# Kernel tuning notes

Hardware: AMD Instinct MI355X
Metric: run time of the kernel (lower is better)

## Reference

```python
import jax, jax.numpy as jnp
import numpy as np

N = 50000      # nodes per type (tx and addr)
E = 400000     # edges per relation
IN, H, OUT = 128, 256, 2
RELS = ['tt', 'aa', 'at', 'ta']


def setup_inputs() -> dict:
    key = jax.random.key(0)
    ks = jax.random.split(key, 32)
    inp = {}
    inp['x_tx'] = jax.random.normal(ks[0], (N, IN), jnp.float32)
    inp['x_addr'] = jax.random.normal(ks[1], (N, IN), jnp.float32)
    for i, r in enumerate(RELS):
        inp['e_' + r] = jax.random.randint(ks[2 + i], (2, E), 0, N, jnp.int32)
    k = 6
    for li, (din, dout) in enumerate([(IN, H), (H, OUT)]):
        for r in RELS:
            inp[f'Wl{li}_{r}'] = jax.random.normal(ks[k], (dout, din), jnp.float32) * 0.05; k += 1
            inp[f'bl{li}_{r}'] = jnp.zeros((dout,), jnp.float32)
            inp[f'Wr{li}_{r}'] = jax.random.normal(ks[k], (dout, din), jnp.float32) * 0.05; k += 1
    return inp


def _sage(x_src, x_dst, edge, Wl, bl, Wr):
    # PyG SAGEConv: lin_l(mean_{j in N(i)} x_j) + lin_r(x_i)
    n = x_dst.shape[0]
    msg = x_src[edge[0]]                                         # [E, d] gather
    s = jax.ops.segment_sum(msg, edge[1], num_segments=n)        # [n, d] scatter-add
    cnt = jax.ops.segment_sum(jnp.ones((edge.shape[1],), x_src.dtype), edge[1], num_segments=n)
    agg = s / jnp.maximum(cnt, 1.0)[:, None]                     # mean (0 for isolated)
    return agg @ Wl.T + bl + x_dst @ Wr.T


def reference(x_tx, x_addr, e_tt, e_aa, e_at, e_ta,
              Wl0_tt, bl0_tt, Wr0_tt, Wl0_aa, bl0_aa, Wr0_aa,
              Wl0_at, bl0_at, Wr0_at, Wl0_ta, bl0_ta, Wr0_ta,
              Wl1_tt, bl1_tt, Wr1_tt, Wl1_aa, bl1_aa, Wr1_aa,
              Wl1_at, bl1_at, Wr1_at, Wl1_ta, bl1_ta, Wr1_ta):
    # Layer 0: HeteroConv with aggr='sum' over relations per destination type
    h_tx = _sage(x_tx, x_tx, e_tt, Wl0_tt, bl0_tt, Wr0_tt) + \
           _sage(x_addr, x_tx, e_at, Wl0_at, bl0_at, Wr0_at)
    h_ad = _sage(x_addr, x_addr, e_aa, Wl0_aa, bl0_aa, Wr0_aa) + \
           _sage(x_tx, x_addr, e_ta, Wl0_ta, bl0_ta, Wr0_ta)
    h_tx = jax.nn.relu(h_tx)   # dropout is identity at inference
    h_ad = jax.nn.relu(h_ad)
    # Layer 1 (output)
    o_tx = _sage(h_tx, h_tx, e_tt, Wl1_tt, bl1_tt, Wr1_tt) + \
           _sage(h_ad, h_tx, e_at, Wl1_at, bl1_at, Wr1_at)
    o_ad = _sage(h_ad, h_ad, e_aa, Wl1_aa, bl1_aa, Wr1_aa) + \
           _sage(h_tx, h_ad, e_ta, Wl1_ta, bl1_ta, Wr1_ta)
    return o_tx, o_ad
```

## Files before the change

### kernel.cpp

```cpp
#include <hip/hip_runtime.h>
#include <hip/hip_fp8.h>


#define DIN 128
#define DH  256
#define LDSA 136
#define LDSH 264

typedef __attribute__((ext_vector_type(8))) short bf16x8;
typedef __attribute__((ext_vector_type(4))) float f32x4;
typedef __attribute__((ext_vector_type(2))) float f32x2;

__device__ __forceinline__ unsigned short f2bf(float f) {
    unsigned int u = __float_as_uint(f);
    u = (u + 0x7fffu + ((u >> 16) & 1u)) >> 16;
    return (unsigned short)u;
}

#if __has_builtin(__builtin_amdgcn_cvt_pk_fp8_f32) && __has_builtin(__builtin_amdgcn_cvt_pk_f32_fp8)
__device__ __forceinline__ unsigned pk_fp8(float4 a) {
    unsigned v = (unsigned)__builtin_amdgcn_cvt_pk_fp8_f32(a.x, a.y, 0, false);
    v = (unsigned)__builtin_amdgcn_cvt_pk_fp8_f32(a.z, a.w, (int)v, true);
    return v;
}
__device__ __forceinline__ void acc_fp8x4(float* a, unsigned u) {
    f32x2 f0 = __builtin_amdgcn_cvt_pk_f32_fp8((int)u, false);
    f32x2 f1 = __builtin_amdgcn_cvt_pk_f32_fp8((int)u, true);
    a[0] += f0.x; a[1] += f0.y; a[2] += f1.x; a[3] += f1.y;
}
#else
__device__ __forceinline__ unsigned pk_fp8(float4 a) {
    __hip_fp8_e4m3 v0(a.x), v1(a.y), v2(a.z), v3(a.w);
    return (unsigned)v0.__x | ((unsigned)v1.__x << 8) |
           ((unsigned)v2.__x << 16) | ((unsigned)v3.__x << 24);
}
__device__ __forceinline__ void acc_fp8x4(float* a, unsigned u) {
    __hip_fp8_e4m3 v0, v1, v2, v3;
    v0.__x = (unsigned char)(u & 0xff);
    v1.__x = (unsigned char)((u >> 8) & 0xff);
    v2.__x = (unsigned char)((u >> 16) & 0xff);
    v3.__x = (unsigned char)((u >> 24) & 0xff);
    a[0] += (float)v0; a[1] += (float)v1; a[2] += (float)v2; a[3] += (float)v3;
}
#endif

__device__ __forceinline__ void acc_fp8x16(float* a, uint4 u) {
    acc_fp8x4(a + 0,  u.x);
    acc_fp8x4(a + 4,  u.y);
    acc_fp8x4(a + 8,  u.z);
    acc_fp8x4(a + 12, u.w);
}

__global__ __launch_bounds__(256) void setup_kernel(
    const float* __restrict__ x_tx, const float* __restrict__ x_addr,
    const float* __restrict__ Wl0_tt, const float* __restrict__ Wl0_aa,
    const float* __restrict__ Wl0_at, const float* __restrict__ Wl0_ta,
    const float* __restrict__ Wr0_tt, const float* __restrict__ Wr0_aa,
    const float* __restrict__ Wr0_at, const float* __restrict__ Wr0_ta,
    const float* __restrict__ bl0_tt, const float* __restrict__ bl0_aa,
    const float* __restrict__ bl0_at, const float* __restrict__ bl0_ta,
    const float* __restrict__ Wl1_tt, const float* __restrict__ Wl1_aa,
    const float* __restrict__ Wl1_at, const float* __restrict__ Wl1_ta,
    const float* __restrict__ Wr1_tt, const float* __restrict__ Wr1_aa,
    const float* __restrict__ Wr1_at, const float* __restrict__ Wr1_ta,
    const float* __restrict__ bl1_tt, const float* __restrict__ bl1_aa,
    const float* __restrict__ bl1_at, const float* __restrict__ bl1_ta,
    unsigned short* __restrict__ xb_tx, unsigned short* __restrict__ xb_ad,
    uint2* __restrict__ x8_tx, uint2* __restrict__ x8_ad,
    unsigned short* __restrict__ wb_tt, unsigned short* __restrict__ wb_aa,
    unsigned short* __restrict__ wb_at, unsigned short* __restrict__ wb_ta,
    unsigned short* __restrict__ wr0c_tx, unsigned short* __restrict__ wr0c_ad,
    float* __restrict__ b0c, unsigned short* __restrict__ wzb,
    float* __restrict__ b1c, int N)
{
    int i = blockIdx.x * blockDim.x + threadIdx.x;
    int nconv = N * DIN / 8;
    if (i < nconv) {
        {
            const float4* p = (const float4*)(x_tx + (size_t)i * 8);
            float4 a = p[0], b = p[1];
            uint4 o;
            o.x = (unsigned)f2bf(a.x) | ((unsigned)f2bf(a.y) << 16);
            o.y = (unsigned)f2bf(a.z) | ((unsigned)f2bf(a.w) << 16);
            o.z = (unsigned)f2bf(b.x) | ((unsigned)f2bf(b.y) << 16);
            o.w = (unsigned)f2bf(b.z) | ((unsigned)f2bf(b.w) << 16);
            *(uint4*)(xb_tx + (size_t)i * 8) = o;
            x8_tx[i] = make_uint2(pk_fp8(a), pk_fp8(b));
        }
        {
            const float4* p = (const float4*)(x_addr + (size_t)i * 8);
            float4 a = p[0], b = p[1];
            uint4 o;
            o.x = (unsigned)f2bf(a.x) | ((unsigned)f2bf(a.y) << 16);
            o.y = (unsigned)f2bf(a.z) | ((unsigned)f2bf(a.w) << 16);
            o.z = (unsigned)f2bf(b.x) | ((unsigned)f2bf(b.y) << 16);
            o.w = (unsigned)f2bf(b.z) | ((unsigned)f2bf(b.w) << 16);
            *(uint4*)(xb_ad + (size_t)i * 8) = o;
            x8_ad[i] = make_uint2(pk_fp8(a), pk_fp8(b));
        }
    }
    if (i < DH * DIN) {
        wb_tt[i] = f2bf(Wl0_tt[i]);
        wb_aa[i] = f2bf(Wl0_aa[i]);
        wb_at[i] = f2bf(Wl0_at[i]);
        wb_ta[i] = f2bf(Wl0_ta[i]);
        wr0c_tx[i] = f2bf(Wr0_tt[i] + Wr0_at[i]);
        wr0c_ad[i] = f2bf(Wr0_aa[i] + Wr0_ta[i]);
    }
    if (i < DH) {
        b0c[i]      = bl0_tt[i] + bl0_at[i];
        b0c[DH + i] = bl0_aa[i] + bl0_ta[i];
    }
    if (i < 2 * 16 * DH) {
        int type = i >> 12;
        int rem = i & 4095;
        int r = rem >> 8;
        int c = rem & 255;
        float v = 0.f;
        if (r < 6) {
            const float* A = type ? Wl1_aa : Wl1_tt;
            const float* B = type ? Wl1_at : Wl1_ta;
            if (r == 0) v = A[c];
            else if (r == 1) v = A[DH + c];
            else if (r == 2) v = B[c];
            else if (r == 3) v = B[DH + c];
            else if (r == 4) v = type ? (Wr1_aa[c] + Wr1_ta[c]) : (Wr1_tt[c] + Wr1_at[c]);
            else             v = type ? (Wr1_aa[DH + c] + Wr1_ta[DH + c])
                                      : (Wr1_tt[DH + c] + Wr1_at[DH + c]);
        }
        wzb[i] = f2bf(v);
    }
    if (i < 2) {
        b1c[i]     = bl1_tt[i] + bl1_at[i];
        b1c[2 + i] = bl1_aa[i] + bl1_ta[i];
    }
}

__global__ __launch_bounds__(256) void bhist_kernel(
    const int* __restrict__ e0, const int* __restrict__ e1,
    const int* __restrict__ e2, const int* __restrict__ e3,
    int* __restrict__ bcnt, int E, int nb)
{
    int r = blockIdx.y;
    const int* e = (r == 0) ? e0 : (r == 1) ? e1 : (r == 2) ? e2 : e3;
    __shared__ int h[256];
    if (threadIdx.x < nb) h[threadIdx.x] = 0;
    __syncthreads();
    int base = (blockIdx.x * 256 + threadIdx.x) * 16;
    if (base + 16 <= E) {
        const int4* p = (const int4*)(e + E + base);
        int4 d0 = p[0], d1 = p[1], d2 = p[2], d3 = p[3];
        atomicAdd(&h[(unsigned)d0.x >> 8], 1); atomicAdd(&h[(unsigned)d0.y >> 8], 1);
        atomicAdd(&h[(unsigned)d0.z >> 8], 1); atomicAdd(&h[(unsigned)d0.w >> 8], 1);
        atomicAdd(&h[(unsigned)d1.x >> 8], 1); atomicAdd(&h[(unsigned)d1.y >> 8], 1);
        atomicAdd(&h[(unsigned)d1.z >> 8], 1); atomicAdd(&h[(unsigned)d1.w >> 8], 1);
        atomicAdd(&h[(unsigned)d2.x >> 8], 1); atomicAdd(&h[(unsigned)d2.y >> 8], 1);
        atomicAdd(&h[(unsigned)d2.z >> 8], 1); atomicAdd(&h[(unsigned)d2.w >> 8], 1);
        atomicAdd(&h[(unsigned)d3.x >> 8], 1); atomicAdd(&h[(unsigned)d3.y >> 8], 1);
        atomicAdd(&h[(unsigned)d3.z >> 8], 1); atomicAdd(&h[(unsigned)d3.w >> 8], 1);
    } else {
        for (int i = base; i < E; ++i)
            atomicAdd(&h[(unsigned)e[E + i] >> 8], 1);
    }
    __syncthreads();
    if (threadIdx.x < nb) {
        int v = h[threadIdx.x];
        if (v) atomicAdd(&bcnt[r * nb + threadIdx.x], v);
    }
}

__global__ __launch_bounds__(1024) void bscan_kernel(
    const int* __restrict__ bcnt, int* __restrict__ bbase, int* __restrict__ bcur, int n)
{
    __shared__ int s[1024];
    int t = threadIdx.x;
    int v = (t < n) ? bcnt[t] : 0;
    s[t] = v;
    __syncthreads();
    for (int off = 1; off < 1024; off <<= 1) {
        int x = (t >= off) ? s[t - off] : 0;
        __syncthreads();
        s[t] += x;
        __syncthreads();
    }
    if (t < n) {
        int ex = s[t] - v;
        bbase[t] = ex;
        bcur[t] = ex;
    }
    if (t == 0) bbase[n] = s[1023];
}

__global__ __launch_bounds__(256) void bscatter_kernel(
    const int* __restrict__ e0, const int* __restrict__ e1,
    const int* __restrict__ e2, const int* __restrict__ e3,
    int* __restrict__ bcur, unsigned* __restrict__ tmp, int E, int nb)
{
    int r = blockIdx.y;
    const int* e = (r == 0) ? e0 : (r == 1) ? e1 : (r == 2) ? e2 : e3;
    __shared__ int h[256];
    __shared__ int lbase[256];
    __shared__ int lcur[256];
    if (threadIdx.x < nb) { h[threadIdx.x] = 0; lcur[threadIdx.x] = 0; }
    __syncthreads();
    int base = (blockIdx.x * 256 + threadIdx.x) * 16;
    int dst[16], src[16];
    int cnt16 = 0;
    if (base + 16 <= E) {
        const int4* pd = (const int4*)(e + E + base);
        const int4* ps = (const int4*)(e + base);
#pragma unroll
        for (int j = 0; j < 4; ++j) {
            int4 d = pd[j], s4 = ps[j];
            dst[j * 4 + 0] = d.x; dst[j * 4 + 1] = d.y; dst[j * 4 + 2] = d.z; dst[j * 4 + 3] = d.w;
            src[j * 4 + 0] = s4.x; src[j * 4 + 1] = s4.y; src[j * 4 + 2] = s4.z; src[j * 4 + 3] = s4.w;
        }
        cnt16 = 16;
    } else {
        for (int i = base; i < E; ++i) {
            dst[cnt16] = e[E + i];
            src[cnt16] = e[i];
            ++cnt16;
        }
    }
    for (int j = 0; j < cnt16; ++j)
        atomicAdd(&h[(unsigned)dst[j] >> 8], 1);
    __syncthreads();
    if (threadIdx.x < nb) {
        int c = h[threadIdx.x];
        if (c) lbase[threadIdx.x] = atomicAdd(&bcur[r * nb + threadIdx.x], c);
    }
    __syncthreads();
    for (int j = 0; j < cnt16; ++j) {
        int bk = (unsigned)dst[j] >> 8;
        int rank = atomicAdd(&lcur[bk], 1);
        tmp[lbase[bk] + rank] =
            (((unsigned)dst[j] & 255u) << 16) | (unsigned)src[j];
    }
}

__global__ __launch_bounds__(256) void bgroup_kernel(
    const unsigned* __restrict__ tmp, const int* __restrict__ bbase,
    int* __restrict__ col, int* __restrict__ rowptr, int* __restrict__ cnt,
    int N, int nb)
{
    int b = blockIdx.x;
    int r = blockIdx.y;
    int idx = r * nb + b;
    int lo = bbase[idx], hi = bbase[idx + 1];
    __shared__ int h[256];
    __shared__ int cur[256];
    __shared__ int exs[256];
    int t = threadIdx.x;
    h[t] = 0; cur[t] = 0;
    __syncthreads();
    for (int i = lo + t; i < hi; i += 256)
        atomicAdd(&h[(tmp[i] >> 16) & 255u], 1);
    __syncthreads();
    {
        __shared__ int s[256];
        int v = h[t];
        s[t] = v;
        __syncthreads();
        for (int off = 1; off < 256; off <<= 1) {
            int x = (t >= off) ? s[t - off] : 0;
            __syncthreads();
            s[t] += x;
            __syncthreads();
        }
        exs[t] = s[t] - v;
    }
    __syncthreads();
    int d = b * 256 + t;
    if (d < N) {
        rowptr[r * N + d] = lo + exs[t];
        cnt[r * N + d] = h[t];
    }
    for (int i = lo + t; i < hi; i += 256) {
        unsigned p = tmp[i];
        int fine = (p >> 16) & 255u;
        int rank = atomicAdd(&cur[fine], 1);
        col[lo + exs[fine] + rank] = (int)(p & 0xffffu);
    }
}

__global__ __launch_bounds__(256) void agg_kernel(
    const uint4* __restrict__ x8_tx, const uint4* __restrict__ x8_ad,
    const int* __restrict__ rowptr, const int* __restrict__ cnt,
    const int* __restrict__ col, unsigned short* __restrict__ aggb, int N)
{
    int r = blockIdx.y;
    const uint4* xs = (r == 0 || r == 3) ? x8_tx : x8_ad;
    int t = threadIdx.x;
    int wv = t >> 6;
    int l  = t & 63;
    int oct = l >> 3;
    int d   = l & 7;
    int node = blockIdx.x * 32 + wv * 8 + oct;
    if (node >= N) return;
    int idx = r * N + node;
    int base = rowptr[idx];
    int c    = cnt[idx];
    const int* cl = col + base;
    float a0[16] = {}, a1[16] = {};
    int e = 0;
    for (; e + 2 <= c; e += 2) {
        int s0 = cl[e];
        int s1 = cl[e + 1];
        uint4 u0 = xs[((unsigned)s0 << 3) + d];
        uint4 u1 = xs[((unsigned)s1 << 3) + d];
        acc_fp8x16(a0, u0);
        acc_fp8x16(a1, u1);
    }
    if (e < c) {
        int s0 = cl[e];
        uint4 u0 = xs[((unsigned)s0 << 3) + d];
        acc_fp8x16(a0, u0);
    }
    float sc = 1.0f / fmaxf((float)c, 1.0f);
    uint4 o0, o1;
    o0.x = (unsigned)f2bf((a0[0] + a1[0]) * sc)  | ((unsigned)f2bf((a0[1] + a1[1]) * sc) << 16);
    o0.y = (unsigned)f2bf((a0[2] + a1[2]) * sc)  | ((unsigned)f2bf((a0[3] + a1[3]) * sc) << 16);
    o0.z = (unsigned)f2bf((a0[4] + a1[4]) * sc)  | ((unsigned)f2bf((a0[5] + a1[5]) * sc) << 16);
    o0.w = (unsigned)f2bf((a0[6] + a1[6]) * sc)  | ((unsigned)f2bf((a0[7] + a1[7]) * sc) << 16);
    o1.x = (unsigned)f2bf((a0[8] + a1[8]) * sc)  | ((unsigned)f2bf((a0[9] + a1[9]) * sc) << 16);
    o1.y = (unsigned)f2bf((a0[10] + a1[10]) * sc) | ((unsigned)f2bf((a0[11] + a1[11]) * sc) << 16);
    o1.z = (unsigned)f2bf((a0[12] + a1[12]) * sc) | ((unsigned)f2bf((a0[13] + a1[13]) * sc) << 16);
    o1.w = (unsigned)f2bf((a0[14] + a1[14]) * sc) | ((unsigned)f2bf((a0[15] + a1[15]) * sc) << 16);
    uint4* orow = (uint4*)(aggb + ((size_t)r * N + node) * DIN);
    orow[d * 2]     = o0;
    orow[d * 2 + 1] = o1;
}

__global__ __launch_bounds__(256) void gemm0z_kernel(
    const unsigned short* __restrict__ xb_tx, const unsigned short* __restrict__ xb_ad,
    const unsigned short* __restrict__ aggb,
    const unsigned short* __restrict__ wb_tt, const unsigned short* __restrict__ wb_at,
    const unsigned short* __restrict__ wr0c_tx,
    const unsigned short* __restrict__ wb_aa, const unsigned short* __restrict__ wb_ta,
    const unsigned short* __restrict__ wr0c_ad,
    const float* __restrict__ b0c, const unsigned short* __restrict__ wzb,
    const float* __restrict__ b1c,
    float* __restrict__ z, float* __restrict__ outp, int N)
{
    __shared__ unsigned short lds[3 * 64 * LDSA];
    const int type = blockIdx.y;
    const unsigned short* xself = type ? xb_ad : xb_tx;
    const unsigned short* A0 = aggb + (size_t)(type ? 1 : 0) * N * DIN;
    const unsigned short* A1 = aggb + (size_t)(type ? 3 : 2) * N * DIN;
    const unsigned short* W0 = type ? wb_aa   : wb_tt;
    const unsigned short* W1 = type ? wb_ta   : wb_at;
    const unsigned short* W2 = type ? wr0c_ad : wr0c_tx;
    const float* bias = b0c + type * DH;
    float* zA = type ? (z + (size_t)1 * N * 2) : z;
    float* zB = type ? (z + (size_t)2 * N * 2) : (z + (size_t)3 * N * 2);
    float* outSelf = outp + (size_t)type * N * 2;

    const int t  = threadIdx.x;
    const int wv = t >> 6;
    const int l  = t & 63;
    const int q  = l >> 4;
    const int lr = l & 15;
    const int m0 = blockIdx.x * 64;
    const int n0 = wv * 64;

    {
        const uint4* As[3] = {(const uint4*)A0, (const uint4*)A1, (const uint4*)xself};
#pragma unroll
        for (int i = 0; i < 12; ++i) {
            int cid = i * 256 + t;
            int seg = cid >> 10;
            int rem = cid & 1023;
            int row = rem >> 4;
            int ch  = rem & 15;
            int gr = m0 + row; if (gr >= N) gr = N - 1;
            uint4 v = As[seg][((unsigned)gr << 4) + ch];
            *(uint4*)&lds[(seg * 64 + row) * LDSA + ch * 8] = v;
        }
    }
    __syncthreads();

    f32x4 accm[4][4] = {};
    {
        const unsigned short* Ws[3] = {W0, W1, W2};
        for (int seg = 0; seg < 3; ++seg) {
            const unsigned short* W = Ws[seg];
            const unsigned short* la = &lds[(seg * 64 + lr) * LDSA + q * 8];
            const unsigned short* pb0 = W + (unsigned)(n0 + lr) * DIN + q * 8;
            const unsigned short* pb1 = W + (unsigned)(n0 + 16 + lr) * DIN + q * 8;
            const unsigned short* pb2 = W + (unsigned)(n0 + 32 + lr) * DIN + q * 8;
            const unsigned short* pb3 = W + (unsigned)(n0 + 48 + lr) * DIN + q * 8;
#pragma unroll
            for (int k = 0; k < DIN; k += 32) {
                bf16x8 b0 = *(const bf16x8*)(pb0 + k);
                bf16x8 b1 = *(const bf16x8*)(pb1 + k);
                bf16x8 b2 = *(const bf16x8*)(pb2 + k);
                bf16x8 b3 = *(const bf16x8*)(pb3 + k);
#pragma unroll
                for (int mt = 0; mt < 4; ++mt) {
                    bf16x8 a = *(const bf16x8*)(la + mt * 16 * LDSA + k);
                    accm[mt][0] = __builtin_amdgcn_mfma_f32_16x16x32_bf16(a, b0, accm[mt][0], 0, 0, 0);
                    accm[mt][1] = __builtin_amdgcn_mfma_f32_16x16x32_bf16(a, b1, accm[mt][1], 0, 0, 0);
                    accm[mt][2] = __builtin_amdgcn_mfma_f32_16x16x32_bf16(a, b2, accm[mt][2], 0, 0, 0);
                    accm[mt][3] = __builtin_amdgcn_mfma_f32_16x16x32_bf16(a, b3, accm[mt][3], 0, 0, 0);
                }
            }
        }
    }
    __syncthreads();

    {
        float bias_nt[4];
#pragma unroll
        for (int nt = 0; nt < 4; ++nt) bias_nt[nt] = bias[n0 + nt * 16 + lr];
#pragma unroll
        for (int mt = 0; mt < 4; ++mt) {
#pragma unroll
            for (int nt = 0; nt < 4; ++nt) {
                int colc = n0 + nt * 16 + lr;
#pragma unroll
                for (int rr = 0; rr < 4; ++rr) {
                    int row = mt * 16 + q * 4 + rr;
                    lds[row * LDSH + colc] =
                        f2bf(fmaxf(accm[mt][nt][rr] + bias_nt[nt], 0.f));
                }
            }
        }
    }
    __syncthreads();

    {
        const unsigned short* wz = wzb + (size_t)type * 16 * DH;
        f32x4 az = {};
        const unsigned short* la = &lds[(wv * 16 + lr) * LDSH + q * 8];
        const unsigned short* pb = wz + lr * DH + q * 8;
#pragma unroll
        for (int k = 0; k < DH; k += 32) {
            bf16x8 a = *(const bf16x8*)(la + k);
            bf16x8 b = *(const bf16x8*)(pb + k);
            az = __builtin_amdgcn_mfma_f32_16x16x32_bf16(a, b, az, 0, 0, 0);
        }
        if (lr < 6) {
#pragma unroll
            for (int reg = 0; reg < 4; ++reg) {
                int node = m0 + wv * 16 + q * 4 + reg;
                if (node < N) {
                    float v = az[reg];
                    if (lr < 2)      zA[node * 2 + lr] = v;
                    else if (lr < 4) zB[node * 2 + lr - 2] = v;
                    else             outSelf[node * 2 + lr - 4] = v + b1c[type * 2 + lr - 4];
                }
            }
        }
    }
}

__global__ __launch_bounds__(256) void l1_agg_kernel(
    const int* __restrict__ rowptr, const int* __restrict__ cnt, const int* __restrict__ col,
    const float* __restrict__ z, float* __restrict__ out, int N)
{
    const int type = blockIdx.y;
    const int rA = type ? 1 : 0;
    const int rB = type ? 3 : 2;
    const float* zAp = type ? (z + (size_t)1 * N * 2) : z;
    const float* zBp = type ? (z + (size_t)3 * N * 2) : (z + (size_t)2 * N * 2);
    float* outp = out + (size_t)type * N * 2;

    const int t = threadIdx.x;
    const int wave = t >> 6;
    const int l = t & 63;
    const int sub = l >> 3;
    const int es  = l & 7;
    int node = blockIdx.x * 32 + wave * 8 + sub;
    bool valid = node < N;

    float ax = 0.f, ay = 0.f;
#pragma unroll
    for (int ri = 0; ri < 2; ++ri) {
        int rel = ri ? rB : rA;
        const float* zp = ri ? zBp : zAp;
        int b = 0, c = 0;
        if (valid) { b = rowptr[rel * N + node]; c = cnt[rel * N + node]; }
        const int* cl = col + b;
        float sx = 0.f, sy = 0.f;
        for (int e = es; e < c; e += 8) {
            int s = cl[e];
            float2 v = *(const float2*)(zp + (size_t)s * 2);
            sx += v.x; sy += v.y;
        }
        sx += __shfl_xor(sx, 1, 64); sy += __shfl_xor(sy, 1, 64);
        sx += __shfl_xor(sx, 2, 64); sy += __shfl_xor(sy, 2, 64);
        sx += __shfl_xor(sx, 4, 64); sy += __shfl_xor(sy, 4, 64);
        float sc = 1.0f / fmaxf((float)c, 1.0f);
        ax += sx * sc; ay += sy * sc;
    }
    if (valid && es == 0) {
        float2 o = *(float2*)(outp + (size_t)node * 2);
        o.x += ax; o.y += ay;
        *(float2*)(outp + (size_t)node * 2) = o;
    }
}

extern "C" void kernel_launch(void* const* d_in, const int* in_sizes, int n_in,
                              void* d_out, int out_size, void* d_ws, size_t ws_size,
                              hipStream_t stream)
{
    const float* x_tx   = (const float*)d_in[0];
    const float* x_addr = (const float*)d_in[1];
    const int* e_tt = (const int*)d_in[2];
    const int* e_aa = (const int*)d_in[3];
    const int* e_at = (const int*)d_in[4];
    const int* e_ta = (const int*)d_in[5];
    const float* Wl0_tt = (const float*)d_in[6];
    const float* bl0_tt = (const float*)d_in[7];
    const float* Wr0_tt = (const float*)d_in[8];
    const float* Wl0_aa = (const float*)d_in[9];
    const float* bl0_aa = (const float*)d_in[10];
    const float* Wr0_aa = (const float*)d_in[11];
    const float* Wl0_at = (const float*)d_in[12];
    const float* bl0_at = (const float*)d_in[13];
    const float* Wr0_at = (const float*)d_in[14];
    const float* Wl0_ta = (const float*)d_in[15];
    const float* bl0_ta = (const float*)d_in[16];
    const float* Wr0_ta = (const float*)d_in[17];
    const float* Wl1_tt = (const float*)d_in[18];
    const float* bl1_tt = (const float*)d_in[19];
    const float* Wr1_tt = (const float*)d_in[20];
    const float* Wl1_aa = (const float*)d_in[21];
    const float* bl1_aa = (const float*)d_in[22];
    const float* Wr1_aa = (const float*)d_in[23];
    const float* Wl1_at = (const float*)d_in[24];
    const float* bl1_at = (const float*)d_in[25];
    const float* Wr1_at = (const float*)d_in[26];
    const float* Wl1_ta = (const float*)d_in[27];
    const float* bl1_ta = (const float*)d_in[28];
    const float* Wr1_ta = (const float*)d_in[29];

    const int N = in_sizes[0] / DIN;
    const int E = in_sizes[2] / 2;
    const int nb = (N + 255) >> 8;

    size_t off = 0;
    char* base = (char*)d_ws;
    auto alloc = [&](size_t bytes) -> void* {
        void* p = base + off;
        off += (bytes + 255) & ~(size_t)255;
        return p;
    };
    int*   bcnt   = (int*)  alloc((size_t)4 * nb * 4);
    int*   bbase  = (int*)  alloc(((size_t)4 * nb + 1) * 4);
    int*   bcur   = (int*)  alloc((size_t)4 * nb * 4);
    unsigned* tmp = (unsigned*)alloc((size_t)4 * E * 4);
    int*   col    = (int*)  alloc((size_t)4 * E * 4);
    int*   rowptr = (int*)  alloc((size_t)4 * N * 4);
    int*   cnt    = (int*)  alloc((size_t)4 * N * 4);
    unsigned short* xb_tx = (unsigned short*)alloc((size_t)N * DIN * 2);
    unsigned short* xb_ad = (unsigned short*)alloc((size_t)N * DIN * 2);
    uint2* x8_tx = (uint2*)alloc((size_t)N * DIN);
    uint2* x8_ad = (uint2*)alloc((size_t)N * DIN);
    unsigned short* aggb  = (unsigned short*)alloc((size_t)4 * N * DIN * 2);
    float* z      = (float*)alloc((size_t)4 * N * 2 * 4);
    unsigned short* wb_tt  = (unsigned short*)alloc((size_t)DH * DIN * 2);
    unsigned short* wb_aa  = (unsigned short*)alloc((size_t)DH * DIN * 2);
    unsigned short* wb_at  = (unsigned short*)alloc((size_t)DH * DIN * 2);
    unsigned short* wb_ta  = (unsigned short*)alloc((size_t)DH * DIN * 2);
    unsigned short* wr0c_tx = (unsigned short*)alloc((size_t)DH * DIN * 2);
    unsigned short* wr0c_ad = (unsigned short*)alloc((size_t)DH * DIN * 2);
    float* b0c    = (float*)alloc((size_t)2 * DH * 4);
    unsigned short* wzb = (unsigned short*)alloc((size_t)2 * 16 * DH * 2);
    float* b1c    = (float*)alloc((size_t)2 * 2 * 4);
    (void)ws_size;

    float* outp = (float*)d_out;

    hipMemsetAsync(bcnt, 0, (size_t)4 * nb * 4, stream);

    {
        int nconv = N * DIN / 8;
        setup_kernel<<<(nconv + 255) / 256, 256, 0, stream>>>(
            x_tx, x_addr,
            Wl0_tt, Wl0_aa, Wl0_at, Wl0_ta,
            Wr0_tt, Wr0_aa, Wr0_at, Wr0_ta,
            bl0_tt, bl0_aa, bl0_at, bl0_ta,
            Wl1_tt, Wl1_aa, Wl1_at, Wl1_ta,
            Wr1_tt, Wr1_aa, Wr1_at, Wr1_ta,
            bl1_tt, bl1_aa, bl1_at, bl1_ta,
            xb_tx, xb_ad, x8_tx, x8_ad,
            wb_tt, wb_aa, wb_at, wb_ta, wr0c_tx, wr0c_ad,
            b0c, wzb, b1c, N);
    }
    {
        dim3 g((E + 4095) / 4096, 4);
        bhist_kernel<<<g, 256, 0, stream>>>(e_tt, e_aa, e_at, e_ta, bcnt, E, nb);
    }
    bscan_kernel<<<1, 1024, 0, stream>>>(bcnt, bbase, bcur, 4 * nb);
    {
        dim3 g((E + 4095) / 4096, 4);
        bscatter_kernel<<<g, 256, 0, stream>>>(e_tt, e_aa, e_at, e_ta, bcur, tmp, E, nb);
    }
    {
        dim3 g(nb, 4);
        bgroup_kernel<<<g, 256, 0, stream>>>(tmp, bbase, col, rowptr, cnt, N, nb);
    }
    {
        dim3 g((N + 31) / 32, 4);
        agg_kernel<<<g, 256, 0, stream>>>((const uint4*)x8_tx, (const uint4*)x8_ad,
                                          rowptr, cnt, col, aggb, N);
    }
    {
        dim3 g((N + 63) / 64, 2);
        gemm0z_kernel<<<g, 256, 0, stream>>>(
            xb_tx, xb_ad, aggb,
            wb_tt, wb_at, wr0c_tx, wb_aa, wb_ta, wr0c_ad,
            b0c, wzb, b1c, z, outp, N);
    }
    {
        dim3 g((N + 31) / 32, 2);
        l1_agg_kernel<<<g, 256, 0, stream>>>(rowptr, cnt, col, z, outp, N);
    }
}
```

Baseline: 303.2 us.

## Drop LDS staging in layer-0 GEMM; each wave computes 16 rows × 256 cols in registers

The fused layer-0 GEMM kernel no longer stages A tiles in LDS or writes the hidden activations back to LDS. Each wave now loads its own 16 rows of A straight from global memory and computes the full 256 hidden columns with 16 accumulators. The second-layer projection (6 outputs) is done with scalar FMAs in fp32, followed by cross-lane shuffle reductions, instead of a bf16 MFMA. This removes LDS traffic and barriers, but every wave must now stream all three 256x128 weight matrices from global/L2, and register pressure rises.

```diff
diff --git a/kernel.cpp b/kernel.cpp
--- a/kernel.cpp
+++ b/kernel.cpp
@@ -4,8 +4,6 @@
 
 #define DIN 128
 #define DH  256
-#define LDSA 136
-#define LDSH 264
 
 typedef __attribute__((ext_vector_type(8))) short bf16x8;
 typedef __attribute__((ext_vector_type(4))) float f32x4;
@@ -70,7 +68,7 @@
     unsigned short* __restrict__ wb_tt, unsigned short* __restrict__ wb_aa,
     unsigned short* __restrict__ wb_at, unsigned short* __restrict__ wb_ta,
     unsigned short* __restrict__ wr0c_tx, unsigned short* __restrict__ wr0c_ad,
-    float* __restrict__ b0c, unsigned short* __restrict__ wzb,
+    float* __restrict__ b0c, float* __restrict__ wzp,
     float* __restrict__ b1c, int N)
 {
     int i = blockIdx.x * blockDim.x + threadIdx.x;
@@ -111,24 +109,22 @@
         b0c[i]      = bl0_tt[i] + bl0_at[i];
         b0c[DH + i] = bl0_aa[i] + bl0_ta[i];
     }
-    if (i < 2 * 16 * DH) {
-        int type = i >> 12;
-        int rem = i & 4095;
-        int r = rem >> 8;
-        int c = rem & 255;
-        float v = 0.f;
-        if (r < 6) {
-            const float* A = type ? Wl1_aa : Wl1_tt;
-            const float* B = type ? Wl1_at : Wl1_ta;
-            if (r == 0) v = A[c];
-            else if (r == 1) v = A[DH + c];
-            else if (r == 2) v = B[c];
-            else if (r == 3) v = B[DH + c];
-            else if (r == 4) v = type ? (Wr1_aa[c] + Wr1_ta[c]) : (Wr1_tt[c] + Wr1_at[c]);
-            else             v = type ? (Wr1_aa[DH + c] + Wr1_ta[DH + c])
-                                      : (Wr1_tt[DH + c] + Wr1_at[DH + c]);
-        }
-        wzb[i] = f2bf(v);
+    if (i < 2 * DH) {
+        int type = i >> 8;
+        int c = i & 255;
+        const float* A = type ? Wl1_aa : Wl1_tt;
+        const float* B = type ? Wl1_at : Wl1_ta;
+        float v4 = type ? (Wr1_aa[c] + Wr1_ta[c]) : (Wr1_tt[c] + Wr1_at[c]);
+        float v5 = type ? (Wr1_aa[DH + c] + Wr1_ta[DH + c])
+                        : (Wr1_tt[DH + c] + Wr1_at[DH + c]);
+        int nt = c >> 4, lr = c & 15;
+        float* wp = wzp + ((size_t)((type * 16 + nt) * 16 + lr)) * 6;
+        wp[0] = A[c];
+        wp[1] = A[DH + c];
+        wp[2] = B[c];
+        wp[3] = B[DH + c];
+        wp[4] = v4;
+        wp[5] = v5;
     }
     if (i < 2) {
         b1c[i]     = bl1_tt[i] + bl1_at[i];
@@ -339,11 +335,10 @@
     const unsigned short* __restrict__ wr0c_tx,
     const unsigned short* __restrict__ wb_aa, const unsigned short* __restrict__ wb_ta,
     const unsigned short* __restrict__ wr0c_ad,
-    const float* __restrict__ b0c, const unsigned short* __restrict__ wzb,
+    const float* __restrict__ b0c, const float* __restrict__ wzp,
     const float* __restrict__ b1c,
     float* __restrict__ z, float* __restrict__ outp, int N)
 {
-    __shared__ unsigned short lds[3 * 64 * LDSA];
     const int type = blockIdx.y;
     const unsigned short* xself = type ? xb_ad : xb_tx;
     const unsigned short* A0 = aggb + (size_t)(type ? 1 : 0) * N * DIN;
@@ -361,95 +356,70 @@
     const int l  = t & 63;
     const int q  = l >> 4;
     const int lr = l & 15;
-    const int m0 = blockIdx.x * 64;
-    const int n0 = wv * 64;
-
-    {
-        const uint4* As[3] = {(const uint4*)A0, (const uint4*)A1, (const uint4*)xself};
-#pragma unroll
-        for (int i = 0; i < 12; ++i) {
-            int cid = i * 256 + t;
-            int seg = cid >> 10;
-            int rem = cid & 1023;
-            int row = rem >> 4;
-            int ch  = rem & 15;
-            int gr = m0 + row; if (gr >= N) gr = N - 1;
-            uint4 v = As[seg][((unsigned)gr << 4) + ch];
-            *(uint4*)&lds[(seg * 64 + row) * LDSA + ch * 8] = v;
-        }
-    }
-    __syncthreads();
-
-    f32x4 accm[4][4] = {};
-    {
+    const int m  = blockIdx.x * 64 + wv * 16;
+    int ra = m + lr; if (ra >= N) ra = N - 1;
+
+    float biasv[16];
+#pragma unroll
+    for (int nt = 0; nt < 16; ++nt) biasv[nt] = bias[nt * 16 + lr];
+
+    f32x4 acc[16] = {};
+    {
+        const unsigned short* As[3] = {A0, A1, xself};
         const unsigned short* Ws[3] = {W0, W1, W2};
         for (int seg = 0; seg < 3; ++seg) {
-            const unsigned short* W = Ws[seg];
-            const unsigned short* la = &lds[(seg * 64 + lr) * LDSA + q * 8];
-            const unsigned short* pb0 = W + (unsigned)(n0 + lr) * DIN + q * 8;
-            const unsigned short* pb1 = W + (unsigned)(n0 + 16 + lr) * DIN + q * 8;
-            const unsigned short* pb2 = W + (unsigned)(n0 + 32 + lr) * DIN + q * 8;
-            const unsigned short* pb3 = W + (unsigned)(n0 + 48 + lr) * DIN + q * 8;
+            const unsigned short* pa = As[seg] + (unsigned)ra * DIN + q * 8;
+            const unsigned short* pw = Ws[seg] + (unsigned)lr * DIN + q * 8;
 #pragma unroll
             for (int k = 0; k < DIN; k += 32) {
-                bf16x8 b0 = *(const bf16x8*)(pb0 + k);
-                bf16x8 b1 = *(const bf16x8*)(pb1 + k);
-                bf16x8 b2 = *(const bf16x8*)(pb2 + k);
-                bf16x8 b3 = *(const bf16x8*)(pb3 + k);
-#pragma unroll
-                for (int mt = 0; mt < 4; ++mt) {
-                    bf16x8 a = *(const bf16x8*)(la + mt * 16 * LDSA + k);
-                    accm[mt][0] = __builtin_amdgcn_mfma_f32_16x16x32_bf16(a, b0, accm[mt][0], 0, 0, 0);
-                    accm[mt][1] = __builtin_amdgcn_mfma_f32_16x16x32_bf16(a, b1, accm[mt][1], 0, 0, 0);
-                    accm[mt][2] = __builtin_amdgcn_mfma_f32_16x16x32_bf16(a, b2, accm[mt][2], 0, 0, 0);
-                    accm[mt][3] = __builtin_amdgcn_mfma_f32_16x16x32_bf16(a, b3, accm[mt][3], 0, 0, 0);
+                bf16x8 a = *(const bf16x8*)(pa + k);
+#pragma unroll
+                for (int nt = 0; nt < 16; ++nt) {
+                    bf16x8 b = *(const bf16x8*)(pw + (unsigned)nt * 16 * DIN + k);
+                    acc[nt] = __builtin_amdgcn_mfma_f32_16x16x32_bf16(a, b, acc[nt], 0, 0, 0);
                 }
             }
         }
     }
-    __syncthreads();
-
-    {
-        float bias_nt[4];
-#pragma unroll
-        for (int nt = 0; nt < 4; ++nt) bias_nt[nt] = bias[n0 + nt * 16 + lr];
-#pragma unroll
-        for (int mt = 0; mt < 4; ++mt) {
-#pragma unroll
-            for (int nt = 0; nt < 4; ++nt) {
-                int colc = n0 + nt * 16 + lr;
-#pragma unroll
-                for (int rr = 0; rr < 4; ++rr) {
-                    int row = mt * 16 + q * 4 + rr;
-                    lds[row * LDSH + colc] =
-                        f2bf(fmaxf(accm[mt][nt][rr] + bias_nt[nt], 0.f));
-                }
+
+    float p[6][4] = {};
+    {
+        const float* wzt = wzp + (size_t)type * 16 * 16 * 6 + (size_t)lr * 6;
+#pragma unroll
+        for (int nt = 0; nt < 16; ++nt) {
+            const float* wv6 = wzt + (size_t)nt * 16 * 6;
+            float w0 = wv6[0], w1 = wv6[1], w2 = wv6[2];
+            float w3 = wv6[3], w4 = wv6[4], w5 = wv6[5];
+#pragma unroll
+            for (int rr = 0; rr < 4; ++rr) {
+                float h = fmaxf(acc[nt][rr] + biasv[nt], 0.f);
+                p[0][rr] += h * w0; p[1][rr] += h * w1; p[2][rr] += h * w2;
+                p[3][rr] += h * w3; p[4][rr] += h * w4; p[5][rr] += h * w5;
             }
         }
     }
-    __syncthreads();
-
-    {
-        const unsigned short* wz = wzb + (size_t)type * 16 * DH;
-        f32x4 az = {};
-        const unsigned short* la = &lds[(wv * 16 + lr) * LDSH + q * 8];
-        const unsigned short* pb = wz + lr * DH + q * 8;
-#pragma unroll
-        for (int k = 0; k < DH; k += 32) {
-            bf16x8 a = *(const bf16x8*)(la + k);
-            bf16x8 b = *(const bf16x8*)(pb + k);
-            az = __builtin_amdgcn_mfma_f32_16x16x32_bf16(a, b, az, 0, 0, 0);
-        }
-        if (lr < 6) {
-#pragma unroll
-            for (int reg = 0; reg < 4; ++reg) {
-                int node = m0 + wv * 16 + q * 4 + reg;
-                if (node < N) {
-                    float v = az[reg];
-                    if (lr < 2)      zA[node * 2 + lr] = v;
-                    else if (lr < 4) zB[node * 2 + lr - 2] = v;
-                    else             outSelf[node * 2 + lr - 4] = v + b1c[type * 2 + lr - 4];
-                }
+#pragma unroll
+    for (int j = 0; j < 6; ++j) {
+#pragma unroll
+        for (int rr = 0; rr < 4; ++rr) {
+            p[j][rr] += __shfl_xor(p[j][rr], 1, 64);
+            p[j][rr] += __shfl_xor(p[j][rr], 2, 64);
+            p[j][rr] += __shfl_xor(p[j][rr], 4, 64);
+            p[j][rr] += __shfl_xor(p[j][rr], 8, 64);
+        }
+    }
+    if (lr == 0) {
+        float bz0 = b1c[type * 2], bz1 = b1c[type * 2 + 1];
+#pragma unroll
+        for (int rr = 0; rr < 4; ++rr) {
+            int node = m + q * 4 + rr;
+            if (node < N) {
+                zA[node * 2]     = p[0][rr];
+                zA[node * 2 + 1] = p[1][rr];
+                zB[node * 2]     = p[2][rr];
+                zB[node * 2 + 1] = p[3][rr];
+                outSelf[node * 2]     = p[4][rr] + bz0;
+                outSelf[node * 2 + 1] = p[5][rr] + bz1;
             }
         }
     }
@@ -567,7 +537,7 @@
     unsigned short* wr0c_tx = (unsigned short*)alloc((size_t)DH * DIN * 2);
     unsigned short* wr0c_ad = (unsigned short*)alloc((size_t)DH * DIN * 2);
     float* b0c    = (float*)alloc((size_t)2 * DH * 4);
-    unsigned short* wzb = (unsigned short*)alloc((size_t)2 * 16 * DH * 2);
+    float* wzp    = (float*)alloc((size_t)2 * 16 * 16 * 6 * 4);
     float* b1c    = (float*)alloc((size_t)2 * 2 * 4);
     (void)ws_size;
 
@@ -587,7 +557,7 @@
             bl1_tt, bl1_aa, bl1_at, bl1_ta,
             xb_tx, xb_ad, x8_tx, x8_ad,
             wb_tt, wb_aa, wb_at, wb_ta, wr0c_tx, wr0c_ad,
-            b0c, wzb, b1c, N);
+            b0c, wzp, b1c, N);
     }
     {
         dim3 g((E + 4095) / 4096, 4);
@@ -612,7 +582,7 @@
         gemm0z_kernel<<<g, 256, 0, stream>>>(
             xb_tx, xb_ad, aggb,
             wb_tt, wb_at, wr0c_tx, wb_aa, wb_ta, wr0c_ad,
-            b0c, wzb, b1c, z, outp, N);
+            b0c, wzp, b1c, z, outp, N);
     }
     {
         dim3 g((N + 31) / 32, 2);
```

Result: slower. 419.0 us (+38.2%).

## Fuse layer-1 projection into GEMM epilogue via register dot products

Applied to the files above, without the earlier changes.

The second-layer projection (256->6 outputs) was done by staging the relu'd hidden tile as bf16 in LDS and running a small MFMA pass. It is now computed directly from the accumulator registers: each lane multiplies its hidden values by fp32 weights, reduces across 16 lanes with xor shuffles, and accumulates per-row partials into a small LDS buffer with shared atomics. This removes the LDS write and read of the hidden tile, one barrier, and the bf16 rounding of hidden activations. In exchange it adds many shuffles and LDS atomics per block, which may cost more than the removed MFMA pass.

```diff
diff --git a/kernel.cpp b/kernel.cpp
--- a/kernel.cpp
+++ b/kernel.cpp
@@ -5,7 +5,6 @@
 #define DIN 128
 #define DH  256
 #define LDSA 136
-#define LDSH 264
 
 typedef __attribute__((ext_vector_type(8))) short bf16x8;
 typedef __attribute__((ext_vector_type(4))) float f32x4;
@@ -70,7 +69,7 @@
     unsigned short* __restrict__ wb_tt, unsigned short* __restrict__ wb_aa,
     unsigned short* __restrict__ wb_at, unsigned short* __restrict__ wb_ta,
     unsigned short* __restrict__ wr0c_tx, unsigned short* __restrict__ wr0c_ad,
-    float* __restrict__ b0c, unsigned short* __restrict__ wzb,
+    float* __restrict__ b0c, float* __restrict__ wzp,
     float* __restrict__ b1c, int N)
 {
     int i = blockIdx.x * blockDim.x + threadIdx.x;
@@ -111,24 +110,22 @@
         b0c[i]      = bl0_tt[i] + bl0_at[i];
         b0c[DH + i] = bl0_aa[i] + bl0_ta[i];
     }
-    if (i < 2 * 16 * DH) {
-        int type = i >> 12;
-        int rem = i & 4095;
-        int r = rem >> 8;
-        int c = rem & 255;
-        float v = 0.f;
-        if (r < 6) {
-            const float* A = type ? Wl1_aa : Wl1_tt;
-            const float* B = type ? Wl1_at : Wl1_ta;
-            if (r == 0) v = A[c];
-            else if (r == 1) v = A[DH + c];
-            else if (r == 2) v = B[c];
-            else if (r == 3) v = B[DH + c];
-            else if (r == 4) v = type ? (Wr1_aa[c] + Wr1_ta[c]) : (Wr1_tt[c] + Wr1_at[c]);
-            else             v = type ? (Wr1_aa[DH + c] + Wr1_ta[DH + c])
-                                      : (Wr1_tt[DH + c] + Wr1_at[DH + c]);
-        }
-        wzb[i] = f2bf(v);
+    if (i < 2 * DH) {
+        int type = i >> 8;
+        int c = i & 255;
+        const float* A = type ? Wl1_aa : Wl1_tt;
+        const float* B = type ? Wl1_at : Wl1_ta;
+        float v4 = type ? (Wr1_aa[c] + Wr1_ta[c]) : (Wr1_tt[c] + Wr1_at[c]);
+        float v5 = type ? (Wr1_aa[DH + c] + Wr1_ta[DH + c])
+                        : (Wr1_tt[DH + c] + Wr1_at[DH + c]);
+        int cg = c >> 4, lr = c & 15;
+        float* wp = wzp + ((size_t)((type * 16 + cg) * 16 + lr)) * 6;
+        wp[0] = A[c];
+        wp[1] = A[DH + c];
+        wp[2] = B[c];
+        wp[3] = B[DH + c];
+        wp[4] = v4;
+        wp[5] = v5;
     }
     if (i < 2) {
         b1c[i]     = bl1_tt[i] + bl1_at[i];
@@ -339,11 +336,12 @@
     const unsigned short* __restrict__ wr0c_tx,
     const unsigned short* __restrict__ wb_aa, const unsigned short* __restrict__ wb_ta,
     const unsigned short* __restrict__ wr0c_ad,
-    const float* __restrict__ b0c, const unsigned short* __restrict__ wzb,
+    const float* __restrict__ b0c, const float* __restrict__ wzp,
     const float* __restrict__ b1c,
     float* __restrict__ z, float* __restrict__ outp, int N)
 {
     __shared__ unsigned short lds[3 * 64 * LDSA];
+    __shared__ float zacc[64 * 6];
     const int type = blockIdx.y;
     const unsigned short* xself = type ? xb_ad : xb_tx;
     const unsigned short* A0 = aggb + (size_t)(type ? 1 : 0) * N * DIN;
@@ -377,6 +375,8 @@
             uint4 v = As[seg][((unsigned)gr << 4) + ch];
             *(uint4*)&lds[(seg * 64 + row) * LDSA + ch * 8] = v;
         }
+        zacc[t] = 0.f;
+        if (t < 128) zacc[256 + t] = 0.f;
     }
     __syncthreads();
 
@@ -407,22 +407,50 @@
             }
         }
     }
-    __syncthreads();
 
     {
         float bias_nt[4];
-#pragma unroll
-        for (int nt = 0; nt < 4; ++nt) bias_nt[nt] = bias[n0 + nt * 16 + lr];
+        float wzr[4][6];
+#pragma unroll
+        for (int nt = 0; nt < 4; ++nt) {
+            bias_nt[nt] = bias[n0 + nt * 16 + lr];
+            const float* wp = wzp + ((size_t)((type * 16 + (wv * 4 + nt)) * 16 + lr)) * 6;
+#pragma unroll
+            for (int j = 0; j < 6; ++j) wzr[nt][j] = wp[j];
+        }
 #pragma unroll
         for (int mt = 0; mt < 4; ++mt) {
+            float p[6][4] = {};
 #pragma unroll
             for (int nt = 0; nt < 4; ++nt) {
-                int colc = n0 + nt * 16 + lr;
+#pragma unroll
+                for (int rr = 0; rr < 4; ++rr) {
+                    float h = fmaxf(accm[mt][nt][rr] + bias_nt[nt], 0.f);
+                    p[0][rr] += h * wzr[nt][0];
+                    p[1][rr] += h * wzr[nt][1];
+                    p[2][rr] += h * wzr[nt][2];
+                    p[3][rr] += h * wzr[nt][3];
+                    p[4][rr] += h * wzr[nt][4];
+                    p[5][rr] += h * wzr[nt][5];
+                }
+            }
+#pragma unroll
+            for (int j = 0; j < 6; ++j) {
+#pragma unroll
+                for (int rr = 0; rr < 4; ++rr) {
+                    p[j][rr] += __shfl_xor(p[j][rr], 1, 64);
+                    p[j][rr] += __shfl_xor(p[j][rr], 2, 64);
+                    p[j][rr] += __shfl_xor(p[j][rr], 4, 64);
+                    p[j][rr] += __shfl_xor(p[j][rr], 8, 64);
+                }
+            }
+            if (lr == 0) {
 #pragma unroll
                 for (int rr = 0; rr < 4; ++rr) {
                     int row = mt * 16 + q * 4 + rr;
-                    lds[row * LDSH + colc] =
-                        f2bf(fmaxf(accm[mt][nt][rr] + bias_nt[nt], 0.f));
+#pragma unroll
+                    for (int j = 0; j < 6; ++j)
+                        atomicAdd(&zacc[row * 6 + j], p[j][rr]);
                 }
             }
         }
@@ -430,26 +458,19 @@
     __syncthreads();
 
     {
-        const unsigned short* wz = wzb + (size_t)type * 16 * DH;
-        f32x4 az = {};
-        const unsigned short* la = &lds[(wv * 16 + lr) * LDSH + q * 8];
-        const unsigned short* pb = wz + lr * DH + q * 8;
-#pragma unroll
-        for (int k = 0; k < DH; k += 32) {
-            bf16x8 a = *(const bf16x8*)(la + k);
-            bf16x8 b = *(const bf16x8*)(pb + k);
-            az = __builtin_amdgcn_mfma_f32_16x16x32_bf16(a, b, az, 0, 0, 0);
-        }
-        if (lr < 6) {
-#pragma unroll
-            for (int reg = 0; reg < 4; ++reg) {
-                int node = m0 + wv * 16 + q * 4 + reg;
-                if (node < N) {
-                    float v = az[reg];
-                    if (lr < 2)      zA[node * 2 + lr] = v;
-                    else if (lr < 4) zB[node * 2 + lr - 2] = v;
-                    else             outSelf[node * 2 + lr - 4] = v + b1c[type * 2 + lr - 4];
-                }
+        float bz0 = b1c[type * 2], bz1 = b1c[type * 2 + 1];
+#pragma unroll
+        for (int e = t; e < 384; e += 256) {
+            int row = e / 6, j = e % 6;
+            int node = m0 + row;
+            if (node < N) {
+                float v = zacc[e];
+                if (j == 0)      zA[node * 2] = v;
+                else if (j == 1) zA[node * 2 + 1] = v;
+                else if (j == 2) zB[node * 2] = v;
+                else if (j == 3) zB[node * 2 + 1] = v;
+                else if (j == 4) outSelf[node * 2] = v + bz0;
+                else             outSelf[node * 2 + 1] = v + bz1;
             }
         }
     }
@@ -567,7 +588,7 @@
     unsigned short* wr0c_tx = (unsigned short*)alloc((size_t)DH * DIN * 2);
     unsigned short* wr0c_ad = (unsigned short*)alloc((size_t)DH * DIN * 2);
     float* b0c    = (float*)alloc((size_t)2 * DH * 4);
-    unsigned short* wzb = (unsigned short*)alloc((size_t)2 * 16 * DH * 2);
+    float* wzp    = (float*)alloc((size_t)2 * 16 * 16 * 6 * 4);
     float* b1c    = (float*)alloc((size_t)2 * 2 * 4);
     (void)ws_size;
 
@@ -587,7 +608,7 @@
             bl1_tt, bl1_aa, bl1_at, bl1_ta,
             xb_tx, xb_ad, x8_tx, x8_ad,
             wb_tt, wb_aa, wb_at, wb_ta, wr0c_tx, wr0c_ad,
-            b0c, wzb, b1c, N);
+            b0c, wzp, b1c, N);
     }
     {
         dim3 g((E + 4095) / 4096, 4);
@@ -612,7 +633,7 @@
         gemm0z_kernel<<<g, 256, 0, stream>>>(
             xb_tx, xb_ad, aggb,
             wb_tt, wb_at, wr0c_tx, wb_aa, wb_ta, wr0c_ad,
-            b0c, wzb, b1c, z, outp, N);
+            b0c, wzp, b1c, z, outp, N);
     }
     {
         dim3 g((N + 31) / 32, 2);
```

Measured after the change: 347.6 us. +14.6%, slower.
